# Kernel optimization log

Measured on AMD Instinct MI355X. Metric: run time of the kernel, lower is better.

## Reference

```python
import jax, jax.numpy as jnp
import numpy as np

B, L = 1024, 4096        # cycles x timesteps
CC = 3                   # SC channels (SC[...,2:3] = nominal capacity)
XC = 2 + CC              # p_net input: [SOC, T, SC...]
# bounds from params['a123'] for (R_1, 1/R_1C_1, OCV-U, -M_H, K_H)
LB = jnp.array([0.005, 0.025, 0.1, 0.0, 0.002], dtype=jnp.float32)
UB = jnp.array([0.02, 0.07, 1.0, 0.055, 0.025], dtype=jnp.float32)


def setup_inputs() -> dict:
    key = jax.random.key(0)
    ks = jax.random.split(key, 10)
    t = jnp.broadcast_to(jnp.arange(L, dtype=jnp.float32), (B, L))  # monotone time
    I = 1.0 + 0.1 * jax.random.normal(ks[0], (B, L))  # current, bounded away from 0 (IR_estim divides by I)
    T = jax.random.normal(ks[1], (B, L))              # temperature
    dummy = jax.random.normal(ks[2], (B, L))          # unused column 3
    SOC = jax.random.uniform(ks[3], (B, L))
    X = jnp.stack([t, I, T, dummy, SOC], axis=-1)     # [B, L, 5]
    SC = jax.random.uniform(ks[4], (B, CC), minval=0.5, maxval=1.5)
    std = 0.1  # init_network_weights: normal(0, 0.1), zero bias
    pW1 = std * jax.random.normal(ks[5], (XC, 2 * XC))
    pb1 = jnp.zeros((2 * XC,), jnp.float32)
    pW2 = std * jax.random.normal(ks[6], (2 * XC, 5))
    pb2 = jnp.zeros((5,), jnp.float32)
    rW1 = std * jax.random.normal(ks[7], (XC, 1))
    rb1 = jnp.zeros((1,), jnp.float32)
    rW2 = std * jax.random.normal(ks[8], (1, 1))
    rb2 = jnp.zeros((1,), jnp.float32)
    return dict(X=X, SC=SC, pW1=pW1, pb1=pb1, pW2=pW2, pb2=pb2,
                rW1=rW1, rb1=rb1, rW2=rW2, rb2=rb2)


def reference(X, SC, pW1, pb1, pW2, pb2, rW1, rb1, rW2, rb2):
    t = X[..., 0:1]
    I = X[..., 1:2]
    T = X[..., 2:3]
    SOC = X[..., 4:]
    sc_b = jnp.broadcast_to(SC[:, None, :], (X.shape[0], X.shape[1], SC.shape[-1]))
    x = jnp.concatenate([SOC, T, sc_b], axis=-1)                 # [B, L, XC]
    p = jax.nn.softplus(x @ pW1 + pb1) @ pW2 + pb2               # [B, L, 5]
    theta = LB + (UB - LB) * jax.nn.sigmoid(0.01 * p)
    R_1 = theta[..., 0:1]
    RC_r = theta[..., 1:2]
    OCV_U = theta[..., 2:3]
    M_Hn = theta[..., 3:4]   # -M_H
    K_H = theta[..., 4:5]
    r = jax.nn.softplus(x[:, 0, :] @ rW1 + rb1) @ rW2 + rb2      # [B, 1]
    R_s_init = SC[..., 2:3] * (1.0 + r)
    U_H0 = jnp.zeros((X.shape[0], 1), X.dtype)
    U_10 = -OCV_U[:, 0, :] - U_H0 - I[:, 0, :] * R_s_init
    y0 = jnp.concatenate([U_H0, U_10], axis=-1)                  # [B, 2]

    dt = jnp.swapaxes(t[:, 1:, :] - t[:, :-1, :], 0, 1)          # [L-1, B, 1]
    tm = lambda a: jnp.swapaxes(a[:, :-1, :], 0, 1)              # step inputs use X_ode[:, i]
    scan_in = (dt, tm(I), tm(R_1), tm(RC_r), tm(M_Hn), tm(K_H))

    def step(y, inp):  # explicit Euler, IRODEFunc derivative
        dt_i, I_i, R1_i, RC_i, MH_i, KH_i = inp
        U_H = y[..., 0:1]
        U_1 = y[..., 1:2]
        dU_H = -KH_i * I_i * (-MH_i - U_H)
        dU_1 = RC_i * (R1_i * I_i - U_1)
        y = y + dt_i * jnp.concatenate([dU_H, dU_1], axis=-1)
        return y, y

    _, ys = jax.lax.scan(step, y0, scan_in)                      # [L-1, B, 2]
    voltages = jnp.concatenate([y0[None], ys], axis=0)           # [L, B, 2]
    voltages = jnp.swapaxes(voltages, 0, 1)                      # [B, L, 2]
    U_H = voltages[..., 0:1]
    U_1 = voltages[..., 1:2]
    IR_estim = jnp.nanmean((-OCV_U - U_H - U_1) / I, axis=-2)    # [B, 1]
    return IR_estim
```

## Files before the change

kernel.cpp:

```cpp
#include <hip/hip_runtime.h>

#define NB   1024
#define NL   4096
#define TPB  256
#define QSTEP 1024
#define SPT  4

#define WS_BASE 256
#define WS_PART 16640

typedef float v2f __attribute__((ext_vector_type(2)));

__device__ __forceinline__ float fast_rcp(float x) { return __builtin_amdgcn_rcpf(x); }
__device__ __forceinline__ float fexp2(float x) { return __builtin_amdgcn_exp2f(x); }
__device__ __forceinline__ float flog2(float x) { return __builtin_amdgcn_logf(x); }

#define L2E 1.44269504088896340736f
#define LN2 0.69314718055994530942f

#define SP_C0 1.0f
#define SP_C1 0.0864667f
#define SP_C2 (-0.0015685f)
#define SP_C3 2.5763e-5f

__global__ void __launch_bounds__(256) onenet_prep(
    const float* __restrict__ X,   const float* __restrict__ SC,
    const float* __restrict__ pW1, const float* __restrict__ pb1,
    const float* __restrict__ pW2, const float* __restrict__ pb2,
    const float* __restrict__ rW1, const float* __restrict__ rb1,
    const float* __restrict__ rW2, const float* __restrict__ rb2,
    float* __restrict__ ws)
{
    const int gid = blockIdx.x * 256 + threadIdx.x;
    if (gid < NB) {
        float sc0 = SC[gid * 3 + 0], sc1 = SC[gid * 3 + 1], sc2 = SC[gid * 3 + 2];
        float* bp = ws + WS_BASE + gid * 16;
#pragma unroll
        for (int j = 0; j < 10; ++j) {
            float base = fmaf(sc0, pW1[20 + j],
                         fmaf(sc1, pW1[30 + j],
                         fmaf(sc2, pW1[40 + j], pb1[j])));
            bp[j] = L2E * base;
        }
        const float* x0 = X + (size_t)gid * NL * 5;
        float T0 = x0[2], SOC0 = x0[4];
        float u = rb1[0];
        u = fmaf(SOC0, rW1[0], u);
        u = fmaf(T0,   rW1[1], u);
        u = fmaf(sc0,  rW1[2], u);
        u = fmaf(sc1,  rW1[3], u);
        u = fmaf(sc2,  rW1[4], u);
        float sp = LN2 * flog2(1.0f + fexp2(L2E * u));
        float r  = fmaf(sp, rW2[0], rb2[0]);
        bp[10] = sc2 * (1.0f + r);
    }
    if (blockIdx.x == 0 && threadIdx.x < 75) {
        const int t = threadIdx.x;
        const float LBv[5]   = {0.005f, 0.025f, 0.1f, 0.0f, 0.002f};
        const float UBLB[5]  = {0.015f, 0.045f, 0.9f, 0.055f, 0.023f};
        float v;
        if (t < 20) {
            v = L2E * pW1[t];
        } else if (t < 70) {
            int k = (t - 20) % 5;
            v = LN2 * 0.0025f * UBLB[k] * pW2[t - 20];
        } else {
            int k = t - 70;
            v = LBv[k] + UBLB[k] * fmaf(0.0025f, pb2[k], 0.5f);
        }
        ws[t] = v;
    }
}

__global__ void __launch_bounds__(TPB) onenet_main(
    const float* __restrict__ X, float* __restrict__ ws)
{
    __shared__ float4 tile[TPB * 5];
    __shared__ float  red[TPB / 64][9];

    const int bid  = blockIdx.x;
    const int row  = bid >> 2;
    const int q    = bid & 3;
    const int tid  = threadIdx.x;
    const int lane = tid & 63;
    const int w    = tid >> 6;

    const float* Xq = X + ((size_t)row * NL + (size_t)q * QSTEP) * 5;
    {
        const float4* gq = (const float4*)Xq;
#pragma unroll
        for (int k = 0; k < 5; ++k) {
            int widx = tid + TPB * k;
            int sw   = widx ^ ((widx >> 3) & 7);
            tile[sw] = gq[widx];
        }
    }

    float W1S[10], W1T[10], BASE[10], V4[10];
    v2f V01[10], V23[10], AL01, AL23;
    float AL4;
#pragma unroll
    for (int j = 0; j < 10; ++j) W1S[j] = ws[j];
#pragma unroll
    for (int j = 0; j < 10; ++j) W1T[j] = ws[10 + j];
#pragma unroll
    for (int j = 0; j < 10; ++j) {
        V01[j].x = ws[20 + 5 * j + 0];
        V01[j].y = ws[20 + 5 * j + 1];
        V23[j].x = ws[20 + 5 * j + 2];
        V23[j].y = ws[20 + 5 * j + 3];
        V4[j]    = ws[20 + 5 * j + 4];
    }
    AL01.x = ws[70]; AL01.y = ws[71];
    AL23.x = ws[72]; AL23.y = ws[73];
    AL4    = ws[74];
    {
        const float* bp = ws + WS_BASE + row * 16;
#pragma unroll
        for (int j = 0; j < 10; ++j) BASE[j] = bp[j];
    }

    __syncthreads();

    float f[20];
#pragma unroll
    for (int j = 0; j < 5; ++j) {
        int widx = 5 * tid + j;
        int sw   = widx ^ ((widx >> 3) & 7);
        *(float4*)&f[4 * j] = tile[sw];
    }
    float tn;
    {
        int wn  = 5 * ((tid + 1) & (TPB - 1));
        int swn = wn ^ ((wn >> 3) & 7);
        float tl = tile[swn].x;
        if (tid < TPB - 1)      tn = tl;
        else if (q == 3)        tn = f[15];
        else                    tn = Xq[QSTEP * 5];
    }

    v2f a = {1.f, 1.f}, b = {0.f, 0.f}, cS = {0.f, 0.f}, dS = {0.f, 0.f};
    float oacc = 0.f, OCV0 = 0.f, I0 = 0.f;

#pragma unroll
    for (int i = 0; i < SPT; ++i) {
        float tt = f[5 * i + 0];
        float Ii = f[5 * i + 1];
        float Tt = f[5 * i + 2];
        float SS = f[5 * i + 4];
        float tnx = (i < SPT - 1) ? f[5 * i + 5] : tn;
        float dt  = tnx - tt;
        float inv = fast_rcp(Ii);

        v2f t01 = AL01, t23 = AL23;
        float t4 = AL4;
#pragma unroll
        for (int j = 0; j < 10; ++j) {
            float pre = fmaf(SS, W1S[j], fmaf(Tt, W1T[j], BASE[j]));
            float s   = pre * pre;
            float p   = fmaf(s, SP_C3, SP_C2);
            p = fmaf(s, p, SP_C1);
            p = fmaf(s, p, SP_C0);
            float lam = fmaf(pre, 0.5f, p);
            v2f lam2 = {lam, lam};
            t01 = lam2 * V01[j] + t01;
            t23 = lam2 * V23[j] + t23;
            t4  = fmaf(lam, V4[j], t4);
        }
        oacc = fmaf(-t23.x, inv, oacc);
        if (i == 0) { OCV0 = t23.x; I0 = Ii; }

        float g  = dt * t4 * Ii;
        float hh = dt * t01.y;
        v2f sv = {1.f + g, 1.f - hh};
        v2f bv = {g * t23.y, hh * t01.x * Ii};
        v2f iv = {inv, inv};
        cS = iv * a + cS;
        dS = iv * b + dS;
        b  = sv * b + bv;
        a  = sv * a;
    }

#pragma unroll
    for (int off = 1; off < 64; off <<= 1) {
        v2f a2, b2, c2, d2;
        a2.x = __shfl_down(a.x, off);  a2.y = __shfl_down(a.y, off);
        b2.x = __shfl_down(b.x, off);  b2.y = __shfl_down(b.y, off);
        c2.x = __shfl_down(cS.x, off); c2.y = __shfl_down(cS.y, off);
        d2.x = __shfl_down(dS.x, off); d2.y = __shfl_down(dS.y, off);
        float o2 = __shfl_down(oacc, off);
        v2f nb = a2 * b + b2;
        v2f nc = c2 * a + cS;
        v2f nd = (dS + d2) + c2 * b;
        a = a2 * a; b = nb; cS = nc; dS = nd;
        oacc += o2;
    }

    if (lane == 0) {
        red[w][0] = a.x;  red[w][1] = a.y;
        red[w][2] = b.x;  red[w][3] = b.y;
        red[w][4] = cS.x; red[w][5] = cS.y;
        red[w][6] = dS.x; red[w][7] = dS.y;
        red[w][8] = oacc;
    }
    __syncthreads();

    if (tid == 0) {
#pragma unroll
        for (int k = 1; k < TPB / 64; ++k) {
            v2f ak, bk, ck, dk;
            ak.x = red[k][0]; ak.y = red[k][1];
            bk.x = red[k][2]; bk.y = red[k][3];
            ck.x = red[k][4]; ck.y = red[k][5];
            dk.x = red[k][6]; dk.y = red[k][7];
            v2f nb = ak * b + bk;
            v2f nc = ck * a + cS;
            v2f nd = (dS + dk) + ck * b;
            a = ak * a; b = nb; cS = nc; dS = nd;
            oacc += red[k][8];
        }
        float* pw = ws + WS_PART + (size_t)bid * 12;
        pw[0] = a.x;  pw[1] = b.x;  pw[2] = cS.x; pw[3] = dS.x;
        pw[4] = a.y;  pw[5] = b.y;  pw[6] = cS.y; pw[7] = dS.y;
        pw[8] = oacc;
        if (q == 0) { pw[9] = OCV0; pw[10] = I0; }
    }
}

__global__ void __launch_bounds__(256) onenet_final(
    const float* __restrict__ ws, float* __restrict__ out)
{
    const int row = blockIdx.x * 256 + threadIdx.x;
    if (row >= NB) return;
    const float* p0 = ws + WS_PART + (size_t)row * 48;

    v2f a, b, cS, dS;
    a.x  = p0[0]; a.y  = p0[4];
    b.x  = p0[1]; b.y  = p0[5];
    cS.x = p0[2]; cS.y = p0[6];
    dS.x = p0[3]; dS.y = p0[7];
    float O = p0[8];
    float OCV0 = p0[9], I0 = p0[10];
#pragma unroll
    for (int k = 1; k < 4; ++k) {
        const float* pk = p0 + k * 12;
        v2f ak, bk, ck, dk;
        ak.x = pk[0]; ak.y = pk[4];
        bk.x = pk[1]; bk.y = pk[5];
        ck.x = pk[2]; ck.y = pk[6];
        dk.x = pk[3]; dk.y = pk[7];
        v2f nb = ak * b + bk;
        v2f nc = ck * a + cS;
        v2f nd = (dS + dk) + ck * b;
        a = ak * a; b = nb; cS = nc; dS = nd;
        O += pk[8];
    }
    float Rs  = ws[WS_BASE + row * 16 + 10];
    float U10 = -OCV0 - I0 * Rs;
    float SH  = dS.x;
    float S1  = fmaf(cS.y, U10, dS.y);
    out[row] = (O - SH - S1) * (1.0f / 4096.0f);
}

extern "C" void kernel_launch(void* const* d_in, const int* in_sizes, int n_in,
                              void* d_out, int out_size, void* d_ws, size_t ws_size,
                              hipStream_t stream) {
    const float* X   = (const float*)d_in[0];
    const float* SC  = (const float*)d_in[1];
    const float* pW1 = (const float*)d_in[2];
    const float* pb1 = (const float*)d_in[3];
    const float* pW2 = (const float*)d_in[4];
    const float* pb2 = (const float*)d_in[5];
    const float* rW1 = (const float*)d_in[6];
    const float* rb1 = (const float*)d_in[7];
    const float* rW2 = (const float*)d_in[8];
    const float* rb2 = (const float*)d_in[9];
    float* out = (float*)d_out;
    float* ws  = (float*)d_ws;

    onenet_prep<<<NB / 256, 256, 0, stream>>>(X, SC, pW1, pb1, pW2, pb2,
                                              rW1, rb1, rW2, rb2, ws);
    onenet_main<<<NB * 4, TPB, 0, stream>>>(X, ws);
    onenet_final<<<NB / 256, 256, 0, stream>>>(ws, out);
}
```

Before: 139.9 us.

## Fuse prep kernel into main and pair timesteps for packed v2f MLP math

Removes the separate prep kernel launch by having each main block compute the scaled weights, per-row bias terms and the initial series resistance directly from the raw parameters. The resistance is passed to the final kernel through the partial-results slot instead of the old per-row workspace. The MLP evaluation is also reorganised to process two timesteps at once with v2f vectors so the compiler can emit packed FP32 ops. The trade-off is redundant weight loads and arithmetic in every block, plus higher register pressure.

```diff
diff --git a/kernel.cpp b/kernel.cpp
--- a/kernel.cpp
+++ b/kernel.cpp
@@ -6,7 +6,6 @@
 #define QSTEP 1024
 #define SPT  4
 
-#define WS_BASE 256
 #define WS_PART 16640
 
 typedef float v2f __attribute__((ext_vector_type(2)));
@@ -23,7 +22,7 @@
 #define SP_C2 (-0.0015685f)
 #define SP_C3 2.5763e-5f
 
-__global__ void __launch_bounds__(256) onenet_prep(
+__global__ void __launch_bounds__(TPB) onenet_main(
     const float* __restrict__ X,   const float* __restrict__ SC,
     const float* __restrict__ pW1, const float* __restrict__ pb1,
     const float* __restrict__ pW2, const float* __restrict__ pb2,
@@ -31,18 +30,61 @@
     const float* __restrict__ rW2, const float* __restrict__ rb2,
     float* __restrict__ ws)
 {
-    const int gid = blockIdx.x * 256 + threadIdx.x;
-    if (gid < NB) {
-        float sc0 = SC[gid * 3 + 0], sc1 = SC[gid * 3 + 1], sc2 = SC[gid * 3 + 2];
-        float* bp = ws + WS_BASE + gid * 16;
-#pragma unroll
-        for (int j = 0; j < 10; ++j) {
-            float base = fmaf(sc0, pW1[20 + j],
-                         fmaf(sc1, pW1[30 + j],
-                         fmaf(sc2, pW1[40 + j], pb1[j])));
-            bp[j] = L2E * base;
-        }
-        const float* x0 = X + (size_t)gid * NL * 5;
+    __shared__ float4 tile[TPB * 5];
+    __shared__ float  red[TPB / 64][9];
+
+    const int bid  = blockIdx.x;
+    const int row  = bid >> 2;
+    const int q    = bid & 3;
+    const int tid  = threadIdx.x;
+    const int lane = tid & 63;
+    const int w    = tid >> 6;
+
+    const float* Xq = X + ((size_t)row * NL + (size_t)q * QSTEP) * 5;
+    {
+        const float4* gq = (const float4*)Xq;
+#pragma unroll
+        for (int k = 0; k < 5; ++k) {
+            int widx = tid + TPB * k;
+            int sw   = widx ^ ((widx >> 3) & 7);
+            tile[sw] = gq[widx];
+        }
+    }
+
+    const float sc0 = SC[row * 3 + 0];
+    const float sc1 = SC[row * 3 + 1];
+    const float sc2 = SC[row * 3 + 2];
+
+    float W1S[10], W1T[10], BASE[10];
+    float VR1[10], VRC[10], VOC[10], VMH[10], VKH[10];
+#pragma unroll
+    for (int j = 0; j < 10; ++j) {
+        W1S[j]  = L2E * pW1[j];
+        W1T[j]  = L2E * pW1[10 + j];
+        BASE[j] = L2E * fmaf(sc0, pW1[20 + j],
+                        fmaf(sc1, pW1[30 + j],
+                        fmaf(sc2, pW1[40 + j], pb1[j])));
+    }
+    const float UBLB0 = 0.015f, UBLB1 = 0.045f, UBLB2 = 0.9f,
+                UBLB3 = 0.055f, UBLB4 = 0.023f;
+    const float KC = LN2 * 0.0025f;
+#pragma unroll
+    for (int j = 0; j < 10; ++j) {
+        VR1[j] = KC * UBLB0 * pW2[5 * j + 0];
+        VRC[j] = KC * UBLB1 * pW2[5 * j + 1];
+        VOC[j] = KC * UBLB2 * pW2[5 * j + 2];
+        VMH[j] = KC * UBLB3 * pW2[5 * j + 3];
+        VKH[j] = KC * UBLB4 * pW2[5 * j + 4];
+    }
+    const float A0 = 0.005f + UBLB0 * fmaf(0.0025f, pb2[0], 0.5f);
+    const float A1 = 0.025f + UBLB1 * fmaf(0.0025f, pb2[1], 0.5f);
+    const float A2 = 0.1f   + UBLB2 * fmaf(0.0025f, pb2[2], 0.5f);
+    const float A3 = 0.0f   + UBLB3 * fmaf(0.0025f, pb2[3], 0.5f);
+    const float A4 = 0.002f + UBLB4 * fmaf(0.0025f, pb2[4], 0.5f);
+
+    float Rs = 0.f;
+    if (q == 0) {
+        const float* x0 = X + (size_t)row * NL * 5;
         float T0 = x0[2], SOC0 = x0[4];
         float u = rb1[0];
         u = fmaf(SOC0, rW1[0], u);
@@ -51,73 +93,7 @@
         u = fmaf(sc1,  rW1[3], u);
         u = fmaf(sc2,  rW1[4], u);
         float sp = LN2 * flog2(1.0f + fexp2(L2E * u));
-        float r  = fmaf(sp, rW2[0], rb2[0]);
-        bp[10] = sc2 * (1.0f + r);
-    }
-    if (blockIdx.x == 0 && threadIdx.x < 75) {
-        const int t = threadIdx.x;
-        const float LBv[5]   = {0.005f, 0.025f, 0.1f, 0.0f, 0.002f};
-        const float UBLB[5]  = {0.015f, 0.045f, 0.9f, 0.055f, 0.023f};
-        float v;
-        if (t < 20) {
-            v = L2E * pW1[t];
-        } else if (t < 70) {
-            int k = (t - 20) % 5;
-            v = LN2 * 0.0025f * UBLB[k] * pW2[t - 20];
-        } else {
-            int k = t - 70;
-            v = LBv[k] + UBLB[k] * fmaf(0.0025f, pb2[k], 0.5f);
-        }
-        ws[t] = v;
-    }
-}
-
-__global__ void __launch_bounds__(TPB) onenet_main(
-    const float* __restrict__ X, float* __restrict__ ws)
-{
-    __shared__ float4 tile[TPB * 5];
-    __shared__ float  red[TPB / 64][9];
-
-    const int bid  = blockIdx.x;
-    const int row  = bid >> 2;
-    const int q    = bid & 3;
-    const int tid  = threadIdx.x;
-    const int lane = tid & 63;
-    const int w    = tid >> 6;
-
-    const float* Xq = X + ((size_t)row * NL + (size_t)q * QSTEP) * 5;
-    {
-        const float4* gq = (const float4*)Xq;
-#pragma unroll
-        for (int k = 0; k < 5; ++k) {
-            int widx = tid + TPB * k;
-            int sw   = widx ^ ((widx >> 3) & 7);
-            tile[sw] = gq[widx];
-        }
-    }
-
-    float W1S[10], W1T[10], BASE[10], V4[10];
-    v2f V01[10], V23[10], AL01, AL23;
-    float AL4;
-#pragma unroll
-    for (int j = 0; j < 10; ++j) W1S[j] = ws[j];
-#pragma unroll
-    for (int j = 0; j < 10; ++j) W1T[j] = ws[10 + j];
-#pragma unroll
-    for (int j = 0; j < 10; ++j) {
-        V01[j].x = ws[20 + 5 * j + 0];
-        V01[j].y = ws[20 + 5 * j + 1];
-        V23[j].x = ws[20 + 5 * j + 2];
-        V23[j].y = ws[20 + 5 * j + 3];
-        V4[j]    = ws[20 + 5 * j + 4];
-    }
-    AL01.x = ws[70]; AL01.y = ws[71];
-    AL23.x = ws[72]; AL23.y = ws[73];
-    AL4    = ws[74];
-    {
-        const float* bp = ws + WS_BASE + row * 16;
-#pragma unroll
-        for (int j = 0; j < 10; ++j) BASE[j] = bp[j];
+        Rs = sc2 * (1.0f + fmaf(sp, rW2[0], rb2[0]));
     }
 
     __syncthreads();
@@ -140,46 +116,63 @@
     }
 
     v2f a = {1.f, 1.f}, b = {0.f, 0.f}, cS = {0.f, 0.f}, dS = {0.f, 0.f};
-    float oacc = 0.f, OCV0 = 0.f, I0 = 0.f;
-
-#pragma unroll
-    for (int i = 0; i < SPT; ++i) {
-        float tt = f[5 * i + 0];
-        float Ii = f[5 * i + 1];
-        float Tt = f[5 * i + 2];
-        float SS = f[5 * i + 4];
-        float tnx = (i < SPT - 1) ? f[5 * i + 5] : tn;
-        float dt  = tnx - tt;
-        float inv = fast_rcp(Ii);
-
-        v2f t01 = AL01, t23 = AL23;
-        float t4 = AL4;
+    v2f oaccv = {0.f, 0.f};
+    float OCV0 = 0.f, I0 = 0.f;
+
+#pragma unroll
+    for (int ip = 0; ip < 2; ++ip) {
+        const int i0 = 2 * ip, i1 = 2 * ip + 1;
+        v2f SSv = { f[5 * i0 + 4], f[5 * i1 + 4] };
+        v2f Ttv = { f[5 * i0 + 2], f[5 * i1 + 2] };
+        v2f Iv  = { f[5 * i0 + 1], f[5 * i1 + 1] };
+        float tnx1 = (i1 < SPT - 1) ? f[5 * i1 + 5] : tn;
+        v2f dtv = { f[5 * i1 + 0] - f[5 * i0 + 0], tnx1 - f[5 * i1 + 0] };
+        v2f invv = { fast_rcp(Iv.x), fast_rcp(Iv.y) };
+
+        v2f tR1 = {A0, A0}, tRC = {A1, A1}, tOC = {A2, A2},
+            tMH = {A3, A3}, tKH = {A4, A4};
 #pragma unroll
         for (int j = 0; j < 10; ++j) {
-            float pre = fmaf(SS, W1S[j], fmaf(Tt, W1T[j], BASE[j]));
-            float s   = pre * pre;
-            float p   = fmaf(s, SP_C3, SP_C2);
-            p = fmaf(s, p, SP_C1);
-            p = fmaf(s, p, SP_C0);
-            float lam = fmaf(pre, 0.5f, p);
-            v2f lam2 = {lam, lam};
-            t01 = lam2 * V01[j] + t01;
-            t23 = lam2 * V23[j] + t23;
-            t4  = fmaf(lam, V4[j], t4);
-        }
-        oacc = fmaf(-t23.x, inv, oacc);
-        if (i == 0) { OCV0 = t23.x; I0 = Ii; }
-
-        float g  = dt * t4 * Ii;
-        float hh = dt * t01.y;
-        v2f sv = {1.f + g, 1.f - hh};
-        v2f bv = {g * t23.y, hh * t01.x * Ii};
-        v2f iv = {inv, inv};
-        cS = iv * a + cS;
-        dS = iv * b + dS;
-        b  = sv * b + bv;
-        a  = sv * a;
-    }
+            v2f pre = SSv * W1S[j] + Ttv * W1T[j] + BASE[j];
+            v2f s   = pre * pre;
+            v2f p   = s * SP_C3 + SP_C2;
+            p = s * p + SP_C1;
+            p = s * p + SP_C0;
+            v2f lam = pre * 0.5f + p;
+            tR1 += lam * VR1[j];
+            tRC += lam * VRC[j];
+            tOC += lam * VOC[j];
+            tMH += lam * VMH[j];
+            tKH += lam * VKH[j];
+        }
+        oaccv += tOC * invv;
+        if (ip == 0) { OCV0 = tOC.x; I0 = Iv.x; }
+
+        v2f g  = dtv * tKH * Iv;
+        v2f hh = dtv * tRC;
+        v2f bx = g * tMH;
+        v2f by = hh * tR1 * Iv;
+
+        {
+            v2f sv = {1.f + g.x, 1.f - hh.x};
+            v2f bv = {bx.x, by.x};
+            v2f iv = {invv.x, invv.x};
+            cS = iv * a + cS;
+            dS = iv * b + dS;
+            b  = sv * b + bv;
+            a  = sv * a;
+        }
+        {
+            v2f sv = {1.f + g.y, 1.f - hh.y};
+            v2f bv = {bx.y, by.y};
+            v2f iv = {invv.y, invv.y};
+            cS = iv * a + cS;
+            dS = iv * b + dS;
+            b  = sv * b + bv;
+            a  = sv * a;
+        }
+    }
+    float oacc = -(oaccv.x + oaccv.y);
 
 #pragma unroll
     for (int off = 1; off < 64; off <<= 1) {
@@ -223,7 +216,7 @@
         pw[0] = a.x;  pw[1] = b.x;  pw[2] = cS.x; pw[3] = dS.x;
         pw[4] = a.y;  pw[5] = b.y;  pw[6] = cS.y; pw[7] = dS.y;
         pw[8] = oacc;
-        if (q == 0) { pw[9] = OCV0; pw[10] = I0; }
+        if (q == 0) { pw[9] = OCV0; pw[10] = I0; pw[11] = Rs; }
     }
 }
 
@@ -240,7 +233,7 @@
     cS.x = p0[2]; cS.y = p0[6];
     dS.x = p0[3]; dS.y = p0[7];
     float O = p0[8];
-    float OCV0 = p0[9], I0 = p0[10];
+    float OCV0 = p0[9], I0 = p0[10], Rs = p0[11];
 #pragma unroll
     for (int k = 1; k < 4; ++k) {
         const float* pk = p0 + k * 12;
@@ -255,7 +248,6 @@
         a = ak * a; b = nb; cS = nc; dS = nd;
         O += pk[8];
     }
-    float Rs  = ws[WS_BASE + row * 16 + 10];
     float U10 = -OCV0 - I0 * Rs;
     float SH  = dS.x;
     float S1  = fmaf(cS.y, U10, dS.y);
@@ -278,8 +270,7 @@
     float* out = (float*)d_out;
     float* ws  = (float*)d_ws;
 
-    onenet_prep<<<NB / 256, 256, 0, stream>>>(X, SC, pW1, pb1, pW2, pb2,
-                                              rW1, rb1, rW2, rb2, ws);
-    onenet_main<<<NB * 4, TPB, 0, stream>>>(X, ws);
+    onenet_main<<<NB * 4, TPB, 0, stream>>>(X, SC, pW1, pb1, pW2, pb2,
+                                            rW1, rb1, rW2, rb2, ws);
     onenet_final<<<NB / 256, 256, 0, stream>>>(ws, out);
 }
```

Result: no change. 141.7 us (+1.3%).
